# Performance work log

Hardware: AMD Instinct MI355X
Metric: run time of the kernel (lower is better)

Reference implementation:

```python
import jax, jax.numpy as jnp
import numpy as np

N, E, C, L, NG = 50000, 600000, 128, 7, 512
EPS = 1e-7


def layer_norm(z, g, b):
    mu = z.mean(-1, keepdims=True)
    var = ((z - mu) ** 2).mean(-1, keepdims=True)
    return (z - mu) * jax.lax.rsqrt(var + 1e-5) * g + b


def setup_inputs() -> dict:
    key = jax.random.key(0)
    ks = jax.random.split(key, 16)
    inp = {
        'x': jax.random.randint(ks[0], (N, 9), 0, 64, dtype=jnp.int32),
        'edge_index': jax.random.randint(ks[1], (2, E), 0, N, dtype=jnp.int32),
        'edge_attr': jax.random.randint(ks[2], (E, 3), 0, 8, dtype=jnp.int32),
        'batch': jnp.sort(jax.random.randint(ks[3], (N,), 0, NG, dtype=jnp.int32)),
        'atom_emb': jax.random.normal(ks[4], (9, 64, C), jnp.float32) * 0.1,
        'bond_emb': jax.random.normal(ks[5], (3, 8, C), jnp.float32) * 0.1,
        'vn_emb': jnp.zeros((1, C), jnp.float32),
        'conv_W1': jax.random.normal(ks[6], (L, C, 2 * C), jnp.float32) / np.sqrt(C),
        'conv_b1': jnp.zeros((L, 2 * C), jnp.float32),
        'conv_g1': jnp.ones((L, 2 * C), jnp.float32),
        'conv_bb1': jnp.zeros((L, 2 * C), jnp.float32),
        'conv_W2': jax.random.normal(ks[7], (L, 2 * C, C), jnp.float32) / np.sqrt(2 * C),
        'conv_b2': jnp.zeros((L, C), jnp.float32),
        'norm_g': jnp.ones((L, C), jnp.float32),
        'norm_b': jnp.zeros((L, C), jnp.float32),
        'vn_W1': jax.random.normal(ks[8], (L - 1, C, C), jnp.float32) / np.sqrt(C),
        'vn_b1': jnp.zeros((L - 1, C), jnp.float32),
        'vn_g': jnp.ones((L - 1, C), jnp.float32),
        'vn_bb': jnp.zeros((L - 1, C), jnp.float32),
        'vn_W2': jax.random.normal(ks[9], (L - 1, C, C), jnp.float32) / np.sqrt(C),
        'vn_b2': jnp.zeros((L - 1, C), jnp.float32),
    }
    return inp


def reference(x, edge_index, edge_attr, batch, atom_emb, bond_emb, vn_emb,
              conv_W1, conv_b1, conv_g1, conv_bb1, conv_W2, conv_b2,
              norm_g, norm_b, vn_W1, vn_b1, vn_g, vn_bb, vn_W2, vn_b2):
    src, dst = edge_index[0], edge_index[1]

    # AtomEncoder: sum of per-feature embeddings -> [N, C]
    h = atom_emb[jnp.arange(9), x].sum(axis=1)
    # BondEncoder (conv_encode_edge=False) -> [E, C]
    edge_emb = bond_emb[jnp.arange(3), edge_attr].sum(axis=1)

    # virtual node embedding (one per graph)
    vn = jnp.broadcast_to(vn_emb[0], (NG, C))
    h = h + vn[batch]

    def gen_conv(l, hx):
        # GENConv: msg = relu(x_j + e) + eps; softmax aggregation (t=1); MLP(x+m)
        msg = jax.nn.relu(hx[src] + edge_emb) + EPS                      # [E, C]
        mx = jax.ops.segment_max(msg, dst, num_segments=N)               # [N, C]
        e = jnp.exp(msg - mx[dst])
        den = jax.ops.segment_sum(e, dst, num_segments=N)
        m = jax.ops.segment_sum(msg * (e / (den[dst] + 1e-16)), dst, num_segments=N)
        z = hx + m
        z = jax.nn.relu(layer_norm(z @ conv_W1[l] + conv_b1[l], conv_g1[l], conv_bb1[l]))
        return z @ conv_W2[l] + conv_b2[l]

    # res+ block: Conv -> [Norm -> ReLU -> (VN update) -> Conv + res]*
    h = gen_conv(0, h)
    for l in range(1, L):
        h2 = jax.nn.relu(layer_norm(h, norm_g[l - 1], norm_b[l - 1]))
        vtmp = jax.ops.segment_sum(h2, batch, num_segments=NG) + vn
        v = jax.nn.relu(layer_norm(vtmp @ vn_W1[l - 1] + vn_b1[l - 1], vn_g[l - 1], vn_bb[l - 1]))
        vn = v @ vn_W2[l - 1] + vn_b2[l - 1]
        h2 = h2 + vn[batch]
        h = gen_conv(l, h2) + h
    h = layer_norm(h, norm_g[L - 1], norm_b[L - 1])

    # global_add_pool -> [NG, C]
    return jax.ops.segment_sum(h, batch, num_segments=NG)
```

## Files before the change

kernel.cpp:

```cpp
#include <hip/hip_runtime.h>
#include <hip/hip_bf16.h>
#include <stdint.h>

#define N_NODES 50000
#define N_EDGES 600000
#define CH 128
#define NLAYERS 7
#define NGRAPHS 512

typedef __hip_bfloat16 bf16;
using bf16x8 = __attribute__((ext_vector_type(8))) __bf16;
using f32x4  = __attribute__((ext_vector_type(4))) float;

static __device__ __forceinline__ float b2f(bf16 v){ return __bfloat162float(v); }

__global__ void k_detect(const uint32_t* __restrict__ g, int* __restrict__ flag){
  if (threadIdx.x == 0 && blockIdx.x == 0) flag[0] = (g[0] == 0x3F803F80u) ? 1 : 0;
}

struct Segs { const void* src[12]; float* dst[12]; int n[12]; };

__global__ void k_cvt_all(const int* __restrict__ flag, Segs S){
  int f = flag[0];
  int seg = blockIdx.y;
  int n = S.n[seg];
  const void* src = S.src[seg];
  float* dst = S.dst[seg];
  for (int i = blockIdx.x*blockDim.x + threadIdx.x; i < n; i += gridDim.x*blockDim.x)
    dst[i] = f ? b2f(((const bf16*)src)[i]) : ((const float*)src)[i];
}

__global__ void k_transpose_all(const int* __restrict__ flag,
    const void* W1, const void* W2, const void* vW1, const void* vW2,
    bf16* W1p, bf16* W2T, bf16* vW1p, bf16* vW2T){
  int f = flag[0];
  const int T0 = NLAYERS*128*256, T1 = NLAYERS*256*128;
  const int T2 = (NLAYERS-1)*128*128, T3 = (NLAYERS-1)*128*128;
  int total = T0+T1+T2+T3;
  for (int i = blockIdx.x*blockDim.x + threadIdx.x; i < total; i += gridDim.x*blockDim.x){
    float v; int didx;
    if (i < T0){
      int idx = i; int l = idx/(128*256); int rem = idx - l*128*256; int k = rem >> 8; int n = rem & 255;
      v = f ? b2f(((const bf16*)W1)[idx]) : ((const float*)W1)[idx];
      W1p[(size_t)l*256*136 + n*136 + k] = __float2bfloat16(v);
      continue;
    } else if (i < T0+T1){
      int idx = i-T0; int l = idx/(256*128); int rem = idx - l*256*128; int k = rem >> 7; int n = rem & 127;
      v = f ? b2f(((const bf16*)W2)[idx]) : ((const float*)W2)[idx];
      W2T[(size_t)l*128*256 + n*256 + k] = __float2bfloat16(v);
      continue;
    } else if (i < T0+T1+T2){
      int idx = i-T0-T1; int l = idx/(128*128); int rem = idx - l*128*128; int k = rem >> 7; int n = rem & 127;
      v = f ? b2f(((const bf16*)vW1)[idx]) : ((const float*)vW1)[idx];
      vW1p[(size_t)l*128*136 + n*136 + k] = __float2bfloat16(v);
      continue;
    } else {
      int idx = i-T0-T1-T2; int l = idx/(128*128); int rem = idx - l*128*128; int k = rem >> 7; int n = rem & 127;
      v = f ? b2f(((const bf16*)vW2)[idx]) : ((const float*)vW2)[idx];
      vW2T[(size_t)l*128*128 + n*128 + k] = __float2bfloat16(v);
    }
  }
}

__global__ void k_bondC(const int* __restrict__ flag, const void* __restrict__ bond,
                        float* __restrict__ bondC){
  int f = flag[0];
  int i = blockIdx.x*blockDim.x + threadIdx.x;
  if (i >= 512*128) return;
  int idx = i >> 7, c = i & 127;
  int a0 = idx & 7, a1 = (idx>>3) & 7, a2 = (idx>>6) & 7;
  auto g = [&](int e)->float{ return f ? b2f(((const bf16*)bond)[e]) : ((const float*)bond)[e]; };
  bondC[i] = g((0*8+a0)*128 + c) + g((1*8+a1)*128 + c) + g((2*8+a2)*128 + c);
}

__global__ void k_zero_i32(int* p, int n){
  for (int i = blockIdx.x*blockDim.x + threadIdx.x; i < n; i += gridDim.x*blockDim.x) p[i] = 0;
}

__global__ void k_hist(const int* __restrict__ keys, int* __restrict__ counts, int n){
  for (int i = blockIdx.x*blockDim.x + threadIdx.x; i < n; i += gridDim.x*blockDim.x)
    atomicAdd(&counts[keys[i]], 1);
}

__global__ __launch_bounds__(256) void k_scanA(const int* __restrict__ in, int* __restrict__ out,
                                               int* __restrict__ bsums, int n){
  __shared__ int lds[256];
  int t = threadIdx.x;
  int base = blockIdx.x * 1024;
  int v[4]; int s = 0;
  #pragma unroll
  for (int i=0;i<4;i++){ int idx = base + t*4 + i; int x = (idx<n)? in[idx] : 0; v[i]=x; s+=x; }
  lds[t] = s; __syncthreads();
  for (int off=1; off<256; off<<=1){
    int x = (t>=off)? lds[t-off] : 0;
    __syncthreads();
    lds[t] += x;
    __syncthreads();
  }
  int p = lds[t] - s;
  #pragma unroll
  for (int i=0;i<4;i++){ int idx = base + t*4 + i; if (idx<n) out[idx] = p; p += v[i]; }
  if (t==255) bsums[blockIdx.x] = lds[255];
}

__global__ __launch_bounds__(256) void k_scanB(int* bsums, int nblk){
  __shared__ int lds[256];
  int t = threadIdx.x;
  int v = (t<nblk)? bsums[t] : 0;
  lds[t] = v; __syncthreads();
  for (int off=1; off<256; off<<=1){
    int x = (t>=off)? lds[t-off] : 0;
    __syncthreads();
    lds[t] += x;
    __syncthreads();
  }
  if (t<nblk) bsums[t] = lds[t] - v;
}

__global__ void k_scanC(int* out, const int* bsums, int n){
  for (int i = blockIdx.x*blockDim.x + threadIdx.x; i < n; i += gridDim.x*blockDim.x)
    out[i] += bsums[i >> 10];
}

__global__ void k_scatter(const int* __restrict__ ei, const int* __restrict__ ea,
                          const int* __restrict__ row_ptr, int* __restrict__ fill,
                          uint32_t* __restrict__ csr){
  for (int e = blockIdx.x*blockDim.x + threadIdx.x; e < N_EDGES; e += gridDim.x*blockDim.x){
    int src = ei[e];
    int dst = ei[N_EDGES + e];
    int pos = row_ptr[dst] + atomicAdd(&fill[dst], 1);
    uint32_t a0 = (uint32_t)ea[e*3+0], a1 = (uint32_t)ea[e*3+1], a2 = (uint32_t)ea[e*3+2];
    csr[pos] = (uint32_t)src | ((a0 | (a1<<3) | (a2<<6)) << 16);
  }
}

__global__ void k_gptr(const int* __restrict__ batch, int* __restrict__ gptr){
  int i = blockIdx.x*blockDim.x + threadIdx.x;
  if (i >= N_NODES) return;
  int b = batch[i];
  if (i == 0){ for (int g=0; g<=b; ++g) gptr[g] = 0; }
  else { int bp = batch[i-1]; for (int g=bp+1; g<=b; ++g) gptr[g] = i; }
  if (i == N_NODES-1){ for (int g=b+1; g<=NGRAPHS; ++g) gptr[g] = N_NODES; }
}

__global__ __launch_bounds__(128) void k_atom_encode(const int* __restrict__ x,
    const float* __restrict__ atom_emb, const float* __restrict__ vn_emb,
    uint32_t* __restrict__ hxb){
  int n = blockIdx.x; int c = threadIdx.x;
  float s = vn_emb[c];
  #pragma unroll
  for (int f=0; f<9; ++f){
    int xv = x[n*9+f];
    s += atom_emb[(f*64 + xv)*CH + c];
  }
  float o = __shfl_xor(s, 1);
  if ((c & 1) == 0){
    __hip_bfloat162 p; p.x = __float2bfloat16(s); p.y = __float2bfloat16(o);
    hxb[n*64 + (c>>1)] = *reinterpret_cast<uint32_t*>(&p);
  }
}

__global__ void k_vn_init(const float* __restrict__ vn_emb, float* __restrict__ vn){
  for (int i = blockIdx.x*blockDim.x + threadIdx.x; i < NGRAPHS*CH; i += gridDim.x*blockDim.x)
    vn[i] = vn_emb[i & (CH-1)];
}

__global__ __launch_bounds__(64) void k_aggregate(const uint32_t* __restrict__ hxb,
     const uint32_t* __restrict__ csr, const int* __restrict__ row_ptr,
     const float* __restrict__ bondC, uint32_t* __restrict__ z){
  int n = blockIdx.x; int t = threadIdx.x;
  int s0 = row_ptr[n], s1 = row_ptr[n+1];
  float sa=0.f, sb=0.f, wa=0.f, wb=0.f;
  int i = s0;
  for (; i+4 <= s1; i += 4){
    uint32_t u0=csr[i], u1=csr[i+1], u2=csr[i+2], u3=csr[i+3];
    uint32_t h0 = hxb[(size_t)(u0 & 0xFFFFu)*64 + t];
    uint32_t h1 = hxb[(size_t)(u1 & 0xFFFFu)*64 + t];
    uint32_t h2 = hxb[(size_t)(u2 & 0xFFFFu)*64 + t];
    uint32_t h3 = hxb[(size_t)(u3 & 0xFFFFu)*64 + t];
    float2 c0 = *reinterpret_cast<const float2*>(bondC + (size_t)(u0 >> 16)*128 + 2*t);
    float2 c1 = *reinterpret_cast<const float2*>(bondC + (size_t)(u1 >> 16)*128 + 2*t);
    float2 c2 = *reinterpret_cast<const float2*>(bondC + (size_t)(u2 >> 16)*128 + 2*t);
    float2 c3 = *reinterpret_cast<const float2*>(bondC + (size_t)(u3 >> 16)*128 + 2*t);
    #define EDGE(hp, bc) { \
      float va = __uint_as_float(hp << 16) + bc.x; \
      float vb = __uint_as_float(hp & 0xFFFF0000u) + bc.y; \
      va = fmaxf(va, 0.f) + 1e-7f; vb = fmaxf(vb, 0.f) + 1e-7f; \
      float pa = __expf(va - 10.f), pb = __expf(vb - 10.f); \
      sa += pa; wa += pa*va; sb += pb; wb += pb*vb; }
    EDGE(h0, c0) EDGE(h1, c1) EDGE(h2, c2) EDGE(h3, c3)
  }
  for (; i < s1; ++i){
    uint32_t u = csr[i];
    uint32_t hp = hxb[(size_t)(u & 0xFFFFu)*64 + t];
    float2 bc = *reinterpret_cast<const float2*>(bondC + (size_t)(u >> 16)*128 + 2*t);
    EDGE(hp, bc)
    #undef EDGE
  }
  uint32_t own = hxb[(size_t)n*64 + t];
  float za = __uint_as_float(own << 16)         + wa/(sa + 1e-16f);
  float zb = __uint_as_float(own & 0xFFFF0000u) + wb/(sb + 1e-16f);
  __hip_bfloat162 p; p.x = __float2bfloat16(za); p.y = __float2bfloat16(zb);
  z[(size_t)n*68 + t] = *reinterpret_cast<uint32_t*>(&p);
}

template<int K, int N1, int N2>
__global__ __launch_bounds__(512, 2) void k_mlp5(const bf16* __restrict__ A,
    const bf16* __restrict__ W1p,
    const float* __restrict__ b1, const float* __restrict__ g1, const float* __restrict__ bb1,
    const bf16* __restrict__ W2T,
    const float* __restrict__ b2,
    const float* __restrict__ residual, float* __restrict__ out, int M, int NT)
{
  constexpr int KP  = K + 8;
  constexpr int KK1 = K/32;
  constexpr int WC  = N1/4;
  constexpr int JC  = WC/16;
  constexpr int KK2 = N1/32;
  constexpr int ZTP = N1 + 8;
  constexpr int W1B = N1*KP*2;
  constexpr int AB  = 64*KP*2;
  constexpr int W1CH = W1B/1024;
  constexpr int ACH  = AB/1024;

  __shared__ __align__(16) char smem[W1B + 2*AB + 64*ZTP*2 + 64*4*2*4 + 64*2*4];
  bf16* W1L = (bf16*)smem;
  bf16* Ab0 = (bf16*)(smem + W1B);
  bf16* Ab1 = (bf16*)(smem + W1B + AB);
  bf16* zt  = (bf16*)(smem + W1B + 2*AB);
  float* lnp = (float*)(smem + W1B + 2*AB + 64*ZTP*2);
  float* lnv = (float*)(smem + W1B + 2*AB + 64*ZTP*2 + 2048);

  const int tid = threadIdx.x;
  const int wid = tid >> 6, lane = tid & 63;
  const int wr = wid >> 2, wc = wid & 3;
  const int rlo = lane & 15, hi = lane >> 4, khi = hi*8;

  for (int c = wid; c < W1CH; c += 8)
    __builtin_amdgcn_global_load_lds((const uint32_t*)((const char*)W1p + c*1024 + lane*16),
                                     (uint32_t*)((char*)W1L + c*1024), 16, 0, 0);

  auto stageA = [&](bf16* dst, int tile){
    const char* src = (const char*)A + (size_t)tile*AB;
    for (int c = wid; c < ACH; c += 8)
      __builtin_amdgcn_global_load_lds((const uint32_t*)(src + c*1024 + lane*16),
                                       (uint32_t*)((char*)dst + c*1024), 16, 0, 0);
  };

  int t = blockIdx.x;
  stageA(Ab0, t);
  __syncthreads();
  int cur = 0;

  while (true){
    int tn = t + (int)gridDim.x;
    const bf16* Ac = cur ? Ab1 : Ab0;

    f32x4 acc1[2][JC];
    #pragma unroll
    for (int rt=0;rt<2;++rt)
      #pragma unroll
      for (int jc=0;jc<JC;++jc) acc1[rt][jc] = {0.f,0.f,0.f,0.f};
    #pragma unroll
    for (int kk=0;kk<KK1;++kk){
      bf16x8 af[2], bf_[JC];
      #pragma unroll
      for (int rt=0;rt<2;++rt)
        af[rt] = *reinterpret_cast<const bf16x8*>(Ac + (wr*32 + rt*16 + rlo)*KP + kk*32 + khi);
      #pragma unroll
      for (int jc=0;jc<JC;++jc)
        bf_[jc] = *reinterpret_cast<const bf16x8*>(W1L + (wc*WC + jc*16 + rlo)*KP + kk*32 + khi);
      #pragma unroll
      for (int rt=0;rt<2;++rt)
        #pragma unroll
        for (int jc=0;jc<JC;++jc)
          acc1[rt][jc] = __builtin_amdgcn_mfma_f32_16x16x32_bf16(af[rt], bf_[jc], acc1[rt][jc], 0,0,0);
    }

    float p[2][4], q[2][4];
    #pragma unroll
    for (int rt=0;rt<2;++rt)
      #pragma unroll
      for (int r=0;r<4;++r){ p[rt][r]=0.f; q[rt][r]=0.f; }
    #pragma unroll
    for (int jc=0;jc<JC;++jc){
      float bv = b1[wc*WC + jc*16 + rlo];
      #pragma unroll
      for (int rt=0;rt<2;++rt)
        #pragma unroll
        for (int r=0;r<4;++r){
          float v = acc1[rt][jc][r] + bv; acc1[rt][jc][r] = v;
          p[rt][r] += v; q[rt][r] += v*v;
        }
    }
    #pragma unroll
    for (int rt=0;rt<2;++rt)
      #pragma unroll
      for (int r=0;r<4;++r){
        float pv = p[rt][r], qv = q[rt][r];
        #pragma unroll
        for (int off=1; off<16; off<<=1){ pv += __shfl_xor(pv, off); qv += __shfl_xor(qv, off); }
        if (rlo == 0){
          int row = wr*32 + rt*16 + hi*4 + r;
          lnp[(row*4 + wc)*2 + 0] = pv;
          lnp[(row*4 + wc)*2 + 1] = qv;
        }
      }
    __syncthreads();
    if (tid < 64){
      float P=0.f, Q=0.f;
      #pragma unroll
      for (int w=0;w<4;++w){ P += lnp[(tid*4+w)*2]; Q += lnp[(tid*4+w)*2+1]; }
      float mu = P*(1.f/N1);
      lnv[tid*2]   = mu;
      lnv[tid*2+1] = rsqrtf(Q*(1.f/N1) - mu*mu + 1e-5f);
    }
    __syncthreads();

    #pragma unroll
    for (int rt=0;rt<2;++rt)
      #pragma unroll
      for (int r=0;r<4;++r){
        int row = wr*32 + rt*16 + hi*4 + r;
        float mu = lnv[row*2], rs = lnv[row*2+1];
        #pragma unroll
        for (int jc=0;jc<JC;++jc){
          int col = wc*WC + jc*16 + rlo;
          float y = (acc1[rt][jc][r]-mu)*rs*g1[col] + bb1[col];
          zt[row*ZTP + col] = __float2bfloat16(fmaxf(y, 0.f));
        }
      }
    __syncthreads();

    if (tn < NT) stageA(cur ? Ab0 : Ab1, tn);

    bf16x8 B2f[2][KK2];
    #pragma unroll
    for (int ct=0;ct<2;++ct){
      const bf16* wp = W2T + (size_t)(wc*32 + ct*16 + rlo)*N1 + khi;
      #pragma unroll
      for (int kk=0;kk<KK2;++kk)
        B2f[ct][kk] = *reinterpret_cast<const bf16x8*>(wp + kk*32);
    }
    f32x4 acc2[2][2];
    #pragma unroll
    for (int rt=0;rt<2;++rt)
      #pragma unroll
      for (int ct=0;ct<2;++ct) acc2[rt][ct] = {0.f,0.f,0.f,0.f};
    #pragma unroll
    for (int kk=0;kk<KK2;++kk){
      bf16x8 a2[2];
      #pragma unroll
      for (int rt=0;rt<2;++rt)
        a2[rt] = *reinterpret_cast<const bf16x8*>(zt + (wr*32 + rt*16 + rlo)*ZTP + kk*32 + khi);
      #pragma unroll
      for (int rt=0;rt<2;++rt)
        #pragma unroll
        for (int ct=0;ct<2;++ct)
          acc2[rt][ct] = __builtin_amdgcn_mfma_f32_16x16x32_bf16(a2[rt], B2f[ct][kk], acc2[rt][ct], 0,0,0);
    }
    #pragma unroll
    for (int ct=0;ct<2;++ct){
      int col = wc*32 + ct*16 + rlo;
      float bv = b2[col];
      #pragma unroll
      for (int rt=0;rt<2;++rt)
        #pragma unroll
        for (int r=0;r<4;++r){
          int grow = t*64 + wr*32 + rt*16 + hi*4 + r;
          if (grow < M){
            float v = acc2[rt][ct][r] + bv;
            if (residual) v += residual[(size_t)grow*N2 + col];
            out[(size_t)grow*N2 + col] = v;
          }
        }
    }

    if (tn >= NT) break;
    __syncthreads();
    t = tn; cur ^= 1;
  }
}

__global__ __launch_bounds__(256) void k_ln_row(const float* __restrict__ in,
    const float* __restrict__ g, const float* __restrict__ b,
    float* __restrict__ outF, int rows, int relu)
{
  int wid = threadIdx.x >> 6, lane = threadIdx.x & 63;
  int row = blockIdx.x*4 + wid;
  if (row >= rows) return;
  const float* p = in + (size_t)row*CH;
  float x0 = p[lane], x1 = p[64+lane];
  float s = x0 + x1;
  #pragma unroll
  for (int off=32; off; off>>=1) s += __shfl_xor(s, off);
  float mu = s * (1.0f/CH);
  float d0 = x0-mu, d1 = x1-mu;
  float vs = d0*d0 + d1*d1;
  #pragma unroll
  for (int off=32; off; off>>=1) vs += __shfl_xor(vs, off);
  float rstd = rsqrtf(vs*(1.0f/CH) + 1e-5f);
  float y0 = d0*rstd*g[lane] + b[lane];
  float y1 = d1*rstd*g[64+lane] + b[64+lane];
  if (relu){ y0 = fmaxf(y0,0.f); y1 = fmaxf(y1,0.f); }
  outF[(size_t)row*CH + lane] = y0;
  outF[(size_t)row*CH + 64 + lane] = y1;
}

__global__ void k_vncopy(const float* __restrict__ vn, float* __restrict__ vnacc){
  int i = blockIdx.x*blockDim.x + threadIdx.x;
  if (i < NGRAPHS*CH) vnacc[i] = vn[i];
}

__global__ void k_prep_vtb(const float* __restrict__ vnacc, bf16* __restrict__ vtb){
  int i = blockIdx.x*blockDim.x + threadIdx.x;
  if (i < NGRAPHS*CH) vtb[(i>>7)*136 + (i&127)] = __float2bfloat16(vnacc[i]);
}

#define SEGC 128
__global__ __launch_bounds__(128) void k_segsum2(const float* __restrict__ hx,
    const int* __restrict__ batch, float* __restrict__ vnacc){
  int c = threadIdx.x;
  int n0 = blockIdx.x*SEGC;
  int n1 = n0 + SEGC; if (n1 > N_NODES) n1 = N_NODES;
  if (n0 >= N_NODES) return;
  int cur = batch[n0];
  float s = 0.f;
  for (int n = n0; n < n1; ++n){
    int b = batch[n];
    if (b != cur){ atomicAdd(&vnacc[cur*CH + c], s); s = 0.f; cur = b; }
    s += hx[(size_t)n*CH + c];
  }
  atomicAdd(&vnacc[cur*CH + c], s);
}

__global__ void k_add_vn(const float* __restrict__ hx, const float* __restrict__ vn,
                         const int* __restrict__ batch, uint32_t* __restrict__ hxb){
  for (int i = blockIdx.x*blockDim.x + threadIdx.x; i < N_NODES*64; i += gridDim.x*blockDim.x){
    int n = i >> 6; int t = i & 63;
    float2 hv = *reinterpret_cast<const float2*>(hx + (size_t)n*CH + 2*t);
    float2 vv = *reinterpret_cast<const float2*>(vn + (size_t)batch[n]*CH + 2*t);
    __hip_bfloat162 p; p.x = __float2bfloat16(hv.x+vv.x); p.y = __float2bfloat16(hv.y+vv.y);
    hxb[i] = *reinterpret_cast<uint32_t*>(&p);
  }
}

__global__ __launch_bounds__(128) void k_pool(const float* __restrict__ hx,
    const int* __restrict__ gptr, const int* __restrict__ flag, void* __restrict__ out){
  int g = blockIdx.x; int c = threadIdx.x;
  float s = 0.f;
  for (int n = gptr[g]; n < gptr[g+1]; ++n) s += hx[(size_t)n*CH + c];
  if (flag[0]) ((bf16*)out)[g*CH+c] = __float2bfloat16(s);
  else         ((float*)out)[g*CH+c] = s;
}

extern "C" void kernel_launch(void* const* d_in, const int* in_sizes, int n_in,
                              void* d_out, int out_size, void* d_ws, size_t ws_size,
                              hipStream_t stream)
{
  const int*  x     = (const int*) d_in[0];
  const int*  ei    = (const int*) d_in[1];
  const int*  ea    = (const int*) d_in[2];
  const int*  batch = (const int*) d_in[3];
  const void* atom_emb = d_in[4];
  const void* bond_emb = d_in[5];
  const void* vn_emb   = d_in[6];
  const void* conv_W1  = d_in[7];
  const void* conv_b1  = d_in[8];
  const void* conv_g1  = d_in[9];
  const void* conv_bb1 = d_in[10];
  const void* conv_W2  = d_in[11];
  const void* conv_b2  = d_in[12];
  const void* norm_g   = d_in[13];
  const void* norm_b   = d_in[14];
  const void* vn_W1    = d_in[15];
  const void* vn_b1    = d_in[16];
  const void* vn_g     = d_in[17];
  const void* vn_bb    = d_in[18];
  const void* vn_W2    = d_in[19];
  const void* vn_b2    = d_in[20];

  char* wsb = (char*)d_ws;
  size_t off = 0;
  auto alloc = [&](size_t bytes)->char*{ char* p = wsb + off; off += (bytes + 255) & ~(size_t)255; return p; };
  const int ZROWS = 50048;
  float*    h     = (float*)   alloc(sizeof(float)*N_NODES*CH);
  float*    hx    = (float*)   alloc(sizeof(float)*N_NODES*CH);
  uint32_t* hxb   = (uint32_t*)alloc(sizeof(uint32_t)*N_NODES*64);
  uint32_t* z     = (uint32_t*)alloc(sizeof(uint32_t)*ZROWS*68);
  float*    vn    = (float*)   alloc(sizeof(float)*NGRAPHS*CH);
  float*    vnacc = (float*)   alloc(sizeof(float)*NGRAPHS*CH);
  bf16*     vtb   = (bf16*)    alloc(sizeof(bf16)*NGRAPHS*136);
  bf16*     W1Tp  = (bf16*)    alloc(sizeof(bf16)*NLAYERS*256*136);
  bf16*     W2T   = (bf16*)    alloc(sizeof(bf16)*NLAYERS*128*256);
  bf16*     vW1Tp = (bf16*)    alloc(sizeof(bf16)*(NLAYERS-1)*128*136);
  bf16*     vW2T  = (bf16*)    alloc(sizeof(bf16)*(NLAYERS-1)*128*128);
  int* row_ptr = (int*)alloc(sizeof(int)*(N_NODES+1));
  int* counts  = (int*)alloc(sizeof(int)*(N_NODES+1));
  uint32_t* csr = (uint32_t*)alloc(sizeof(uint32_t)*N_EDGES);
  int* gptr    = (int*)alloc(sizeof(int)*(NGRAPHS+1));
  int* bsums   = (int*)alloc(sizeof(int)*256);
  int* flag    = (int*)alloc(sizeof(int)*64);
  float* atomF = (float*)alloc(sizeof(float)*9*64*CH);
  float* bondC = (float*)alloc(sizeof(float)*512*CH);
  float* vnEF  = (float*)alloc(sizeof(float)*CH);
  float* b1F   = (float*)alloc(sizeof(float)*NLAYERS*2*CH);
  float* g1F   = (float*)alloc(sizeof(float)*NLAYERS*2*CH);
  float* bb1F  = (float*)alloc(sizeof(float)*NLAYERS*2*CH);
  float* b2F   = (float*)alloc(sizeof(float)*NLAYERS*CH);
  float* ngF   = (float*)alloc(sizeof(float)*NLAYERS*CH);
  float* nbF   = (float*)alloc(sizeof(float)*NLAYERS*CH);
  float* vb1F  = (float*)alloc(sizeof(float)*(NLAYERS-1)*CH);
  float* vgF   = (float*)alloc(sizeof(float)*(NLAYERS-1)*CH);
  float* vbbF  = (float*)alloc(sizeof(float)*(NLAYERS-1)*CH);
  float* vb2F  = (float*)alloc(sizeof(float)*(NLAYERS-1)*CH);

  k_detect<<<1, 64, 0, stream>>>((const uint32_t*)norm_g, flag);
  Segs S;
  int si = 0;
  auto seg = [&](const void* s_, float* d_, int n_){ S.src[si]=s_; S.dst[si]=d_; S.n[si]=n_; ++si; };
  seg(atom_emb, atomF, 9*64*CH);
  seg(vn_emb,   vnEF,  CH);
  seg(conv_b1,  b1F,  NLAYERS*2*CH);
  seg(conv_g1,  g1F,  NLAYERS*2*CH);
  seg(conv_bb1, bb1F, NLAYERS*2*CH);
  seg(conv_b2,  b2F,  NLAYERS*CH);
  seg(norm_g,   ngF,  NLAYERS*CH);
  seg(norm_b,   nbF,  NLAYERS*CH);
  seg(vn_b1,    vb1F, (NLAYERS-1)*CH);
  seg(vn_g,     vgF,  (NLAYERS-1)*CH);
  seg(vn_bb,    vbbF, (NLAYERS-1)*CH);
  seg(vn_b2,    vb2F, (NLAYERS-1)*CH);
  k_cvt_all<<<dim3(72, 12), 256, 0, stream>>>(flag, S);
  k_transpose_all<<<640, 256, 0, stream>>>(flag, conv_W1, conv_W2, vn_W1, vn_W2,
                                           W1Tp, W2T, vW1Tp, vW2T);
  k_bondC<<<256, 256, 0, stream>>>(flag, bond_emb, bondC);

  k_zero_i32<<<64, 256, 0, stream>>>(counts, N_NODES+1);
  k_hist<<<512, 256, 0, stream>>>(ei + N_EDGES, counts, N_EDGES);
  int nblkE = (N_NODES+1 + 1023)/1024;
  k_scanA<<<nblkE, 256, 0, stream>>>(counts, row_ptr, bsums, N_NODES+1);
  k_scanB<<<1, 256, 0, stream>>>(bsums, nblkE);
  k_scanC<<<64, 256, 0, stream>>>(row_ptr, bsums, N_NODES+1);
  k_zero_i32<<<64, 256, 0, stream>>>(counts, N_NODES+1);
  k_scatter<<<512, 256, 0, stream>>>(ei, ea, row_ptr, counts, csr);
  k_gptr<<<(N_NODES+255)/256, 256, 0, stream>>>(batch, gptr);

  k_atom_encode<<<N_NODES, 128, 0, stream>>>(x, atomF, vnEF, hxb);
  k_vn_init<<<64, 256, 0, stream>>>(vnEF, vn);

  int lnBlocksN = (N_NODES + 3)/4;
  const int NT_CONV = (N_NODES + 63)/64;
  const int NT_VN   = NGRAPHS/64;

  for (int l = 0; l < NLAYERS; ++l){
    if (l > 0){
      k_ln_row<<<lnBlocksN, 256, 0, stream>>>(h, ngF + (l-1)*CH, nbF + (l-1)*CH, hx, N_NODES, 1);
      k_vncopy<<<(NGRAPHS*CH+255)/256, 256, 0, stream>>>(vn, vnacc);
      k_segsum2<<<(N_NODES+SEGC-1)/SEGC, 128, 0, stream>>>(hx, batch, vnacc);
      k_prep_vtb<<<(NGRAPHS*CH+255)/256, 256, 0, stream>>>(vnacc, vtb);
      k_mlp5<128,128,128><<<NT_VN, 512, 0, stream>>>(vtb,
          vW1Tp + (size_t)(l-1)*128*136, vb1F + (l-1)*CH, vgF + (l-1)*CH, vbbF + (l-1)*CH,
          vW2T + (size_t)(l-1)*128*128, vb2F + (l-1)*CH, nullptr, vn, NGRAPHS, NT_VN);
      k_add_vn<<<1024, 256, 0, stream>>>(hx, vn, batch, hxb);
    }
    k_aggregate<<<N_NODES, 64, 0, stream>>>(hxb, csr, row_ptr, bondC, z);
    k_mlp5<128,256,128><<<256, 512, 0, stream>>>((const bf16*)z,
        W1Tp + (size_t)l*256*136, b1F + l*2*CH, g1F + l*2*CH, bb1F + l*2*CH,
        W2T + (size_t)l*128*256, b2F + l*CH, (l==0)? nullptr : h, h, N_NODES, NT_CONV);
  }
  k_ln_row<<<lnBlocksN, 256, 0, stream>>>(h, ngF + (NLAYERS-1)*CH, nbF + (NLAYERS-1)*CH,
                                          hx, N_NODES, 0);
  k_pool<<<NGRAPHS, 128, 0, stream>>>(hx, gptr, flag, d_out);
}
```

Measured before the change: 1.045 ms.

## Replace padded LDS layouts with XOR swizzle and drop A double-buffering in MLP kernel

Storage for the aggregated features, vn inputs and W1 weights moves from rows padded to 136 elements to unpadded rows whose column index is XOR-swizzled by row, and LDS reads in the fused MLP kernel use the matching swizzle. This avoids bank conflicts without padding and lowers shared memory per block. The kernel also drops double-buffered A staging for a single buffer loaded at the top of each tile. Bias, gamma, beta, W2 fragments and the residual are now loaded into registers ahead of the LayerNorm. Losing the overlap of the next tile's load with compute could expose global-load latency, and the extra registers could lower occupancy.

```diff
diff --git a/kernel.cpp b/kernel.cpp
--- a/kernel.cpp
+++ b/kernel.cpp
@@ -35,25 +35,22 @@
     bf16* W1p, bf16* W2T, bf16* vW1p, bf16* vW2T){
   int f = flag[0];
   const int T0 = NLAYERS*128*256, T1 = NLAYERS*256*128;
-  const int T2 = (NLAYERS-1)*128*128, T3 = (NLAYERS-1)*128*128;
-  int total = T0+T1+T2+T3;
+  const int T2 = (NLAYERS-1)*128*128;
+  int total = T0+T1+2*T2;
   for (int i = blockIdx.x*blockDim.x + threadIdx.x; i < total; i += gridDim.x*blockDim.x){
-    float v; int didx;
+    float v;
     if (i < T0){
       int idx = i; int l = idx/(128*256); int rem = idx - l*128*256; int k = rem >> 8; int n = rem & 255;
       v = f ? b2f(((const bf16*)W1)[idx]) : ((const float*)W1)[idx];
-      W1p[(size_t)l*256*136 + n*136 + k] = __float2bfloat16(v);
-      continue;
+      W1p[(size_t)l*256*128 + n*128 + (k ^ ((n&7)<<3))] = __float2bfloat16(v);
     } else if (i < T0+T1){
       int idx = i-T0; int l = idx/(256*128); int rem = idx - l*256*128; int k = rem >> 7; int n = rem & 127;
       v = f ? b2f(((const bf16*)W2)[idx]) : ((const float*)W2)[idx];
       W2T[(size_t)l*128*256 + n*256 + k] = __float2bfloat16(v);
-      continue;
     } else if (i < T0+T1+T2){
       int idx = i-T0-T1; int l = idx/(128*128); int rem = idx - l*128*128; int k = rem >> 7; int n = rem & 127;
       v = f ? b2f(((const bf16*)vW1)[idx]) : ((const float*)vW1)[idx];
-      vW1p[(size_t)l*128*136 + n*136 + k] = __float2bfloat16(v);
-      continue;
+      vW1p[(size_t)l*128*128 + n*128 + (k ^ ((n&7)<<3))] = __float2bfloat16(v);
     } else {
       int idx = i-T0-T1-T2; int l = idx/(128*128); int rem = idx - l*128*128; int k = rem >> 7; int n = rem & 127;
       v = f ? b2f(((const bf16*)vW2)[idx]) : ((const float*)vW2)[idx];
@@ -201,60 +198,64 @@
   float za = __uint_as_float(own << 16)         + wa/(sa + 1e-16f);
   float zb = __uint_as_float(own & 0xFFFF0000u) + wb/(sb + 1e-16f);
   __hip_bfloat162 p; p.x = __float2bfloat16(za); p.y = __float2bfloat16(zb);
-  z[(size_t)n*68 + t] = *reinterpret_cast<uint32_t*>(&p);
+  z[(size_t)n*64 + (t ^ ((n&7)<<2))] = *reinterpret_cast<uint32_t*>(&p);
 }
 
 template<int K, int N1, int N2>
-__global__ __launch_bounds__(512, 2) void k_mlp5(const bf16* __restrict__ A,
-    const bf16* __restrict__ W1p,
+__global__ __launch_bounds__(512, 2) void k_mlp6(const bf16* __restrict__ A,
+    const bf16* __restrict__ W1s,
     const float* __restrict__ b1, const float* __restrict__ g1, const float* __restrict__ bb1,
     const bf16* __restrict__ W2T,
     const float* __restrict__ b2,
     const float* __restrict__ residual, float* __restrict__ out, int M, int NT)
 {
-  constexpr int KP  = K + 8;
   constexpr int KK1 = K/32;
   constexpr int WC  = N1/4;
   constexpr int JC  = WC/16;
   constexpr int KK2 = N1/32;
-  constexpr int ZTP = N1 + 8;
-  constexpr int W1B = N1*KP*2;
-  constexpr int AB  = 64*KP*2;
-  constexpr int W1CH = W1B/1024;
-  constexpr int ACH  = AB/1024;
-
-  __shared__ __align__(16) char smem[W1B + 2*AB + 64*ZTP*2 + 64*4*2*4 + 64*2*4];
-  bf16* W1L = (bf16*)smem;
-  bf16* Ab0 = (bf16*)(smem + W1B);
-  bf16* Ab1 = (bf16*)(smem + W1B + AB);
-  bf16* zt  = (bf16*)(smem + W1B + 2*AB);
-  float* lnp = (float*)(smem + W1B + 2*AB + 64*ZTP*2);
-  float* lnv = (float*)(smem + W1B + 2*AB + 64*ZTP*2 + 2048);
+  constexpr int W1E = N1*K;
+  constexpr int AE  = 64*K;
+  constexpr int ZE  = 64*N1;
+  __shared__ __align__(16) bf16 W1L[W1E];
+  __shared__ __align__(16) bf16 AL[AE];
+  __shared__ __align__(16) bf16 zt[ZE];
+  __shared__ float lnp[64][4][2];
+  __shared__ float lnv[64][2];
 
   const int tid = threadIdx.x;
   const int wid = tid >> 6, lane = tid & 63;
   const int wr = wid >> 2, wc = wid & 3;
   const int rlo = lane & 15, hi = lane >> 4, khi = hi*8;
 
-  for (int c = wid; c < W1CH; c += 8)
-    __builtin_amdgcn_global_load_lds((const uint32_t*)((const char*)W1p + c*1024 + lane*16),
-                                     (uint32_t*)((char*)W1L + c*1024), 16, 0, 0);
-
-  auto stageA = [&](bf16* dst, int tile){
-    const char* src = (const char*)A + (size_t)tile*AB;
-    for (int c = wid; c < ACH; c += 8)
-      __builtin_amdgcn_global_load_lds((const uint32_t*)(src + c*1024 + lane*16),
-                                       (uint32_t*)((char*)dst + c*1024), 16, 0, 0);
-  };
-
-  int t = blockIdx.x;
-  stageA(Ab0, t);
-  __syncthreads();
-  int cur = 0;
-
-  while (true){
-    int tn = t + (int)gridDim.x;
-    const bf16* Ac = cur ? Ab1 : Ab0;
+  {
+    constexpr int NC_ = (W1E*2)/1024/8;
+    #pragma unroll
+    for (int c=0;c<NC_;++c){
+      int cc = c*8 + wid;
+      __builtin_amdgcn_global_load_lds((const uint32_t*)((const char*)W1s + cc*1024 + lane*16),
+                                       (uint32_t*)((char*)W1L + cc*1024), 16, 0, 0);
+    }
+  }
+  float b1v[JC], gv[JC], bbv[JC];
+  #pragma unroll
+  for (int jc=0;jc<JC;++jc){
+    int col = wc*WC + jc*16 + rlo;
+    b1v[jc] = b1[col]; gv[jc] = g1[col]; bbv[jc] = bb1[col];
+  }
+  float bv2[2] = { b2[wc*32 + rlo], b2[wc*32 + 16 + rlo] };
+
+  for (int t = blockIdx.x; ; ){
+    {
+      const char* src = (const char*)A + (size_t)t*AE*2;
+      constexpr int NCA = (AE*2)/1024/8;
+      #pragma unroll
+      for (int c=0;c<NCA;++c){
+        int cc = c*8 + wid;
+        __builtin_amdgcn_global_load_lds((const uint32_t*)(src + cc*1024 + lane*16),
+                                         (uint32_t*)((char*)AL + cc*1024), 16, 0, 0);
+      }
+    }
+    __syncthreads();
 
     f32x4 acc1[2][JC];
     #pragma unroll
@@ -263,19 +264,45 @@
       for (int jc=0;jc<JC;++jc) acc1[rt][jc] = {0.f,0.f,0.f,0.f};
     #pragma unroll
     for (int kk=0;kk<KK1;++kk){
-      bf16x8 af[2], bf_[JC];
+      bf16x8 af[2], bw[JC];
+      #pragma unroll
+      for (int rt=0;rt<2;++rt){
+        int lr = wr*32 + rt*16 + rlo;
+        af[rt] = *reinterpret_cast<const bf16x8*>(&AL[lr*K + ((kk*32 + khi) ^ ((lr&7)<<3))]);
+      }
+      #pragma unroll
+      for (int jc=0;jc<JC;++jc){
+        int n = wc*WC + jc*16 + rlo;
+        bw[jc] = *reinterpret_cast<const bf16x8*>(&W1L[n*K + ((kk*32 + khi) ^ ((n&7)<<3))]);
+      }
       #pragma unroll
       for (int rt=0;rt<2;++rt)
-        af[rt] = *reinterpret_cast<const bf16x8*>(Ac + (wr*32 + rt*16 + rlo)*KP + kk*32 + khi);
-      #pragma unroll
-      for (int jc=0;jc<JC;++jc)
-        bf_[jc] = *reinterpret_cast<const bf16x8*>(W1L + (wc*WC + jc*16 + rlo)*KP + kk*32 + khi);
+        #pragma unroll
+        for (int jc=0;jc<JC;++jc)
+          acc1[rt][jc] = __builtin_amdgcn_mfma_f32_16x16x32_bf16(af[rt], bw[jc], acc1[rt][jc], 0,0,0);
+    }
+
+    bf16x8 B2f[2][KK2];
+    #pragma unroll
+    for (int ct=0;ct<2;++ct){
+      const bf16* wp = W2T + (size_t)(wc*32 + ct*16 + rlo)*N1 + khi;
+      #pragma unroll
+      for (int kk=0;kk<KK2;++kk)
+        B2f[ct][kk] = *reinterpret_cast<const bf16x8*>(wp + kk*32);
+    }
+    float resv[2][2][4];
+    if (residual){
       #pragma unroll
       for (int rt=0;rt<2;++rt)
         #pragma unroll
-        for (int jc=0;jc<JC;++jc)
-          acc1[rt][jc] = __builtin_amdgcn_mfma_f32_16x16x32_bf16(af[rt], bf_[jc], acc1[rt][jc], 0,0,0);
-    }
+        for (int r=0;r<4;++r){
+          int grow = t*64 + wr*32 + rt*16 + hi*4 + r; if (grow >= M) grow = M-1;
+          #pragma unroll
+          for (int ct=0;ct<2;++ct)
+            resv[rt][ct][r] = residual[(size_t)grow*N2 + wc*32 + ct*16 + rlo];
+        }
+    }
+    __builtin_amdgcn_sched_barrier(0);
 
     float p[2][4], q[2][4];
     #pragma unroll
@@ -283,16 +310,14 @@
       #pragma unroll
       for (int r=0;r<4;++r){ p[rt][r]=0.f; q[rt][r]=0.f; }
     #pragma unroll
-    for (int jc=0;jc<JC;++jc){
-      float bv = b1[wc*WC + jc*16 + rlo];
+    for (int jc=0;jc<JC;++jc)
       #pragma unroll
       for (int rt=0;rt<2;++rt)
         #pragma unroll
         for (int r=0;r<4;++r){
-          float v = acc1[rt][jc][r] + bv; acc1[rt][jc][r] = v;
+          float v = acc1[rt][jc][r] + b1v[jc]; acc1[rt][jc][r] = v;
           p[rt][r] += v; q[rt][r] += v*v;
         }
-    }
     #pragma unroll
     for (int rt=0;rt<2;++rt)
       #pragma unroll
@@ -302,18 +327,17 @@
         for (int off=1; off<16; off<<=1){ pv += __shfl_xor(pv, off); qv += __shfl_xor(qv, off); }
         if (rlo == 0){
           int row = wr*32 + rt*16 + hi*4 + r;
-          lnp[(row*4 + wc)*2 + 0] = pv;
-          lnp[(row*4 + wc)*2 + 1] = qv;
+          lnp[row][wc][0] = pv; lnp[row][wc][1] = qv;
         }
       }
     __syncthreads();
     if (tid < 64){
       float P=0.f, Q=0.f;
       #pragma unroll
-      for (int w=0;w<4;++w){ P += lnp[(tid*4+w)*2]; Q += lnp[(tid*4+w)*2+1]; }
+      for (int w=0;w<4;++w){ P += lnp[tid][w][0]; Q += lnp[tid][w][1]; }
       float mu = P*(1.f/N1);
-      lnv[tid*2]   = mu;
-      lnv[tid*2+1] = rsqrtf(Q*(1.f/N1) - mu*mu + 1e-5f);
+      lnv[tid][0] = mu;
+      lnv[tid][1] = rsqrtf(Q*(1.f/N1) - mu*mu + 1e-5f);
     }
     __syncthreads();
 
@@ -322,26 +346,16 @@
       #pragma unroll
       for (int r=0;r<4;++r){
         int row = wr*32 + rt*16 + hi*4 + r;
-        float mu = lnv[row*2], rs = lnv[row*2+1];
+        float mu = lnv[row][0], rs = lnv[row][1];
         #pragma unroll
         for (int jc=0;jc<JC;++jc){
           int col = wc*WC + jc*16 + rlo;
-          float y = (acc1[rt][jc][r]-mu)*rs*g1[col] + bb1[col];
-          zt[row*ZTP + col] = __float2bfloat16(fmaxf(y, 0.f));
+          float y = (acc1[rt][jc][r]-mu)*rs*gv[jc] + bbv[jc];
+          zt[row*N1 + (col ^ ((row&7)<<3))] = __float2bfloat16(fmaxf(y, 0.f));
         }
       }
     __syncthreads();
 
-    if (tn < NT) stageA(cur ? Ab0 : Ab1, tn);
-
-    bf16x8 B2f[2][KK2];
-    #pragma unroll
-    for (int ct=0;ct<2;++ct){
-      const bf16* wp = W2T + (size_t)(wc*32 + ct*16 + rlo)*N1 + khi;
-      #pragma unroll
-      for (int kk=0;kk<KK2;++kk)
-        B2f[ct][kk] = *reinterpret_cast<const bf16x8*>(wp + kk*32);
-    }
     f32x4 acc2[2][2];
     #pragma unroll
     for (int rt=0;rt<2;++rt)
@@ -351,8 +365,10 @@
     for (int kk=0;kk<KK2;++kk){
       bf16x8 a2[2];
       #pragma unroll
-      for (int rt=0;rt<2;++rt)
-        a2[rt] = *reinterpret_cast<const bf16x8*>(zt + (wr*32 + rt*16 + rlo)*ZTP + kk*32 + khi);
+      for (int rt=0;rt<2;++rt){
+        int row = wr*32 + rt*16 + rlo;
+        a2[rt] = *reinterpret_cast<const bf16x8*>(&zt[row*N1 + ((kk*32 + khi) ^ ((row&7)<<3))]);
+      }
       #pragma unroll
       for (int rt=0;rt<2;++rt)
         #pragma unroll
@@ -360,25 +376,22 @@
           acc2[rt][ct] = __builtin_amdgcn_mfma_f32_16x16x32_bf16(a2[rt], B2f[ct][kk], acc2[rt][ct], 0,0,0);
     }
     #pragma unroll
-    for (int ct=0;ct<2;++ct){
-      int col = wc*32 + ct*16 + rlo;
-      float bv = b2[col];
+    for (int ct=0;ct<2;++ct)
       #pragma unroll
       for (int rt=0;rt<2;++rt)
         #pragma unroll
         for (int r=0;r<4;++r){
           int grow = t*64 + wr*32 + rt*16 + hi*4 + r;
           if (grow < M){
-            float v = acc2[rt][ct][r] + bv;
-            if (residual) v += residual[(size_t)grow*N2 + col];
-            out[(size_t)grow*N2 + col] = v;
+            float v = acc2[rt][ct][r] + bv2[ct];
+            if (residual) v += resv[rt][ct][r];
+            out[(size_t)grow*N2 + wc*32 + ct*16 + rlo] = v;
           }
         }
-    }
-
-    if (tn >= NT) break;
-    __syncthreads();
-    t = tn; cur ^= 1;
+
+    t += (int)gridDim.x;
+    if (t >= NT) break;
+    __syncthreads();
   }
 }
 
@@ -414,7 +427,10 @@
 
 __global__ void k_prep_vtb(const float* __restrict__ vnacc, bf16* __restrict__ vtb){
   int i = blockIdx.x*blockDim.x + threadIdx.x;
-  if (i < NGRAPHS*CH) vtb[(i>>7)*136 + (i&127)] = __float2bfloat16(vnacc[i]);
+  if (i < NGRAPHS*CH){
+    int g = i >> 7, k = i & 127;
+    vtb[g*128 + (k ^ ((g&7)<<3))] = __float2bfloat16(vnacc[i]);
+  }
 }
 
 #define SEGC 128
@@ -487,13 +503,13 @@
   float*    h     = (float*)   alloc(sizeof(float)*N_NODES*CH);
   float*    hx    = (float*)   alloc(sizeof(float)*N_NODES*CH);
   uint32_t* hxb   = (uint32_t*)alloc(sizeof(uint32_t)*N_NODES*64);
-  uint32_t* z     = (uint32_t*)alloc(sizeof(uint32_t)*ZROWS*68);
+  uint32_t* z     = (uint32_t*)alloc(sizeof(uint32_t)*ZROWS*64);
   float*    vn    = (float*)   alloc(sizeof(float)*NGRAPHS*CH);
   float*    vnacc = (float*)   alloc(sizeof(float)*NGRAPHS*CH);
-  bf16*     vtb   = (bf16*)    alloc(sizeof(bf16)*NGRAPHS*136);
-  bf16*     W1Tp  = (bf16*)    alloc(sizeof(bf16)*NLAYERS*256*136);
+  bf16*     vtb   = (bf16*)    alloc(sizeof(bf16)*NGRAPHS*CH);
+  bf16*     W1Tp  = (bf16*)    alloc(sizeof(bf16)*NLAYERS*256*128);
   bf16*     W2T   = (bf16*)    alloc(sizeof(bf16)*NLAYERS*128*256);
-  bf16*     vW1Tp = (bf16*)    alloc(sizeof(bf16)*(NLAYERS-1)*128*136);
+  bf16*     vW1Tp = (bf16*)    alloc(sizeof(bf16)*(NLAYERS-1)*128*128);
   bf16*     vW2T  = (bf16*)    alloc(sizeof(bf16)*(NLAYERS-1)*128*128);
   int* row_ptr = (int*)alloc(sizeof(int)*(N_NODES+1));
   int* counts  = (int*)alloc(sizeof(int)*(N_NODES+1));
@@ -559,14 +575,14 @@
       k_vncopy<<<(NGRAPHS*CH+255)/256, 256, 0, stream>>>(vn, vnacc);
       k_segsum2<<<(N_NODES+SEGC-1)/SEGC, 128, 0, stream>>>(hx, batch, vnacc);
       k_prep_vtb<<<(NGRAPHS*CH+255)/256, 256, 0, stream>>>(vnacc, vtb);
-      k_mlp5<128,128,128><<<NT_VN, 512, 0, stream>>>(vtb,
-          vW1Tp + (size_t)(l-1)*128*136, vb1F + (l-1)*CH, vgF + (l-1)*CH, vbbF + (l-1)*CH,
+      k_mlp6<128,128,128><<<NT_VN, 512, 0, stream>>>(vtb,
+          vW1Tp + (size_t)(l-1)*128*128, vb1F + (l-1)*CH, vgF + (l-1)*CH, vbbF + (l-1)*CH,
           vW2T + (size_t)(l-1)*128*128, vb2F + (l-1)*CH, nullptr, vn, NGRAPHS, NT_VN);
       k_add_vn<<<1024, 256, 0, stream>>>(hx, vn, batch, hxb);
     }
     k_aggregate<<<N_NODES, 64, 0, stream>>>(hxb, csr, row_ptr, bondC, z);
-    k_mlp5<128,256,128><<<256, 512, 0, stream>>>((const bf16*)z,
-        W1Tp + (size_t)l*256*136, b1F + l*2*CH, g1F + l*2*CH, bb1F + l*2*CH,
+    k_mlp6<128,256,128><<<256, 512, 0, stream>>>((const bf16*)z,
+        W1Tp + (size_t)l*256*128, b1F + l*2*CH, g1F + l*2*CH, bb1F + l*2*CH,
         W2T + (size_t)l*128*256, b2F + l*CH, (l==0)? nullptr : h, h, N_NODES, NT_CONV);
   }
   k_ln_row<<<lnBlocksN, 256, 0, stream>>>(h, ngF + (NLAYERS-1)*CH, nbF + (NLAYERS-1)*CH,
```

Measured after the change: 989.6 us. 5.3% less time.
